# Performance work log

Hardware: AMD Instinct MI355X
Metric: run time of the kernel (lower is better)

The kernel has to match this reference:

```python
import jax, jax.numpy as jnp
import numpy as np
from jax import lax

B, C, H, W = 32, 128, 64, 64
K, KH, KW = 4, 3, 3
STRIDE = (1, 1)
PAD = [(1, 1), (1, 1)]


def setup_inputs() -> dict:
    key = jax.random.key(0)
    k1, k2, k3, k4 = jax.random.split(key, 4)
    x = jax.random.normal(k1, (B, C, H, W), dtype=jnp.float32)
    kernels = jax.random.normal(k2, (K, C, C, KH, KW), dtype=jnp.float32)
    fc_w = jax.random.normal(k3, (K, C), dtype=jnp.float32) * (1.0 / np.sqrt(C))
    fc_b = jax.random.normal(k4, (K,), dtype=jnp.float32) * 0.01
    return {"x": x, "kernels": kernels, "fc_w": fc_w, "fc_b": fc_b}


def reference(x, kernels, fc_w, fc_b):
    b, c, h, w = x.shape
    # DynamicRoutingLayer: GAP -> Linear -> sigmoid, then softmax over kernels
    pooled = x.mean(axis=(2, 3))                      # [B, C]
    coeffs = jax.nn.sigmoid(pooled @ fc_w.T + fc_b)   # [B, K]
    coeffs = jax.nn.softmax(coeffs, axis=1)
    # Per-sample mixed kernels: [B, C_out, C_in, kh, kw]
    dyn_k = jnp.einsum('bk,klmij->blmij', coeffs, kernels)
    # Batched per-sample conv via grouped conv: groups = batch
    xg = x.reshape(1, b * c, h, w)
    wg = dyn_k.reshape(b * c, c, KH, KW)
    out = lax.conv_general_dilated(
        xg, wg, window_strides=STRIDE, padding=PAD,
        dimension_numbers=('NCHW', 'OIHW', 'NCHW'),
        feature_group_count=b)
    return out.reshape(b, c, out.shape[2], out.shape[3])
```

## Files before the change

### kernel.cpp

```cpp
#include <hip/hip_runtime.h>
#include <math.h>

typedef __attribute__((ext_vector_type(8))) short s16x8;
typedef __attribute__((ext_vector_type(4))) float f32x4;
typedef __attribute__((ext_vector_type(4))) unsigned int u32x4;

#define CCH 128
#define BSZ 32

static __device__ inline unsigned short f2bf(float f) {
    unsigned u = __float_as_uint(f);
    unsigned r = (u + 0x7FFFu + ((u >> 16) & 1u)) >> 16;
    return (unsigned short)r;
}

static __device__ inline unsigned cvtpk(float lo, float hi) {
    unsigned r;
    asm("v_cvt_pk_bf16_f32 %0, %1, %2" : "=v"(r) : "v"(lo), "v"(hi));
    return r;
}

__global__ __launch_bounds__(256) void pool_kernel(const float* __restrict__ x,
                                                   float* __restrict__ pooled) {
    int blk = blockIdx.x;
    const float4* x4 = (const float4*)(x + (size_t)blk * 4096);
    int t = threadIdx.x;
    float s = 0.f;
#pragma unroll
    for (int j = 0; j < 4; ++j) {
        float4 v = x4[j * 256 + t];
        s += v.x + v.y + v.z + v.w;
    }
#pragma unroll
    for (int off = 32; off; off >>= 1) s += __shfl_xor(s, off, 64);
    __shared__ float red[4];
    if ((t & 63) == 0) red[t >> 6] = s;
    __syncthreads();
    if (t == 0) {
        float tot = red[0] + red[1] + red[2] + red[3];
        pooled[blk] = tot * (1.0f / 4096.0f);
    }
}

__global__ __launch_bounds__(128) void coeff_kernel(const float* __restrict__ pooled,
                                                    const float* __restrict__ fc_w,
                                                    const float* __restrict__ fc_b,
                                                    float* __restrict__ coeffs) {
    int t = threadIdx.x;
    int b = t >> 2, k = t & 3;
    const float4* p4 = (const float4*)(pooled + b * CCH);
    const float4* w4 = (const float4*)(fc_w + k * CCH);
    float dot = fc_b[k];
#pragma unroll
    for (int j = 0; j < 32; ++j) {
        float4 a = p4[j], w = w4[j];
        dot += a.x * w.x + a.y * w.y + a.z * w.z + a.w * w.w;
    }
    float s = 1.0f / (1.0f + expf(-dot));
    float m = s;
    m = fmaxf(m, __shfl_xor(m, 1, 64));
    m = fmaxf(m, __shfl_xor(m, 2, 64));
    float e = expf(s - m);
    float sum = e;
    sum += __shfl_xor(sum, 1, 64);
    sum += __shfl_xor(sum, 2, 64);
    coeffs[t] = e / sum;
}

__global__ __launch_bounds__(256) void mix_kernel(const float* __restrict__ kernels,
                                                  const float* __restrict__ coeffs,
                                                  unsigned short* __restrict__ wmix) {
    extern __shared__ float klds[];
    int bid = blockIdx.x;
    int bq = bid & 15;
    int rest = bid >> 4;
    int cog = rest & 7, cc = rest >> 3;
    int t = threadIdx.x;

    const int KSTR = CCH * CCH * 9;
    for (int s = t; s < 4 * 16 * 288; s += 256) {
        int k = s / 4608;
        int rem = s - k * 4608;
        int co = rem / 288;
        int i = rem - co * 288;
        klds[k * 4624 + co * 289 + i] =
            kernels[(size_t)k * KSTR + ((size_t)(cog * 16 + co) * CCH + cc * 32) * 9 + i];
    }
    __syncthreads();

    int wr = cog >> 2, mt = cog & 3;
#pragma unroll
    for (int jb = 0; jb < 2; ++jb) {
        int b = bq + jb * 16;
        float cf0 = coeffs[b * 4 + 0];
        float cf1 = coeffs[b * 4 + 1];
        float cf2 = coeffs[b * 4 + 2];
        float cf3 = coeffs[b * 4 + 3];
        for (int s = t; s < 576; s += 256) {
            int lane = s & 63;
            int tj = s >> 6;
            int dy = tj / 3, dx = tj - dy * 3;
            int col = lane & 15;
            int ci8 = (lane >> 4) * 8;
            unsigned short vals[8];
#pragma unroll
            for (int e = 0; e < 8; ++e) {
                int idx = col * 289 + (ci8 + e) * 9 + dy * 3 + dx;
                float v = cf0 * klds[idx]
                        + cf1 * klds[4624 + idx]
                        + cf2 * klds[2 * 4624 + idx]
                        + cf3 * klds[3 * 4624 + idx];
                vals[e] = f2bf(v);
            }
            int p = cc * 3 + dy;
            size_t off = (size_t)b * 147456
                       + ((size_t)((p * 3 + dx) * 2 + wr) * 4 + mt) * 512 + (size_t)lane * 8;
            *(s16x8*)&wmix[off] = *(const s16x8*)vals;
        }
    }
}

__global__ __launch_bounds__(512, 4) void conv_kernel(const float* __restrict__ x,
                                                      const unsigned short* __restrict__ wmix,
                                                      float* __restrict__ out) {
    __shared__ unsigned short xs[4 * 66 * 40];

    int bid = blockIdx.x;
    int b = bid & 31, ytile = bid >> 5;
    int y0 = ytile * 2;
    int t = threadIdx.x;
    int l = t & 63, w = t >> 6;
    int wr = w >> 2;
    int wc = (w >> 1) & 1;
    int wn = w & 1;
    int l15 = l & 15, g = l >> 4;

    const unsigned short* wb = wmix + (size_t)b * 147456;

    if (t < 160) {
        int row = t / 40;
        int colsel = (t / 20) & 1;
        int cpart = t % 20;
        *(unsigned*)&xs[(row * 66 + colsel * 65) * 40 + cpart * 2] = 0u;
    }

#pragma unroll
    for (int i = 0; i < 2; ++i) {
        int slot = w + i * 8;
        int row = slot >> 2, colhi = slot & 3;
        int gx = colhi * 16 + l15;
        int gy = y0 + row - 1;
        float v[8];
#pragma unroll
        for (int j = 0; j < 8; ++j) v[j] = 0.f;
        if ((unsigned)gy < 64u) {
            const float* xp = x + (((size_t)b * CCH + g * 8) * 64 + gy) * 64 + gx;
#pragma unroll
            for (int j = 0; j < 8; ++j) v[j] = xp[(size_t)j * 4096];
        }
        unsigned pw[4];
#pragma unroll
        for (int j = 0; j < 4; ++j) pw[j] = cvtpk(v[2 * j], v[2 * j + 1]);
        u32x4 q; q[0] = pw[0]; q[1] = pw[1]; q[2] = pw[2]; q[3] = pw[3];
        *(u32x4*)&xs[(size_t)(row * 66 + gx + 1) * 40 + g * 8] = q;
    }
    __syncthreads();

    f32x4 acc[4][2] = {};
    float xv[2][8];
    unsigned pk[2][4];

    for (int cc = 0; cc < 4; ++cc) {
        s16x8 a[4], n[4];
        {
            const unsigned short* wt = wb + ((size_t)((cc * 3) * 3) * 2 + wr) * 2048 + (size_t)l * 8;
#pragma unroll
            for (int mt = 0; mt < 4; ++mt) a[mt] = *(const s16x8*)(wt + mt * 512);
        }
        if (cc < 3) {
#pragma unroll
            for (int i = 0; i < 2; ++i) {
                int slot = w + i * 8;
                int row = slot >> 2, colhi = slot & 3;
                int gx = colhi * 16 + l15;
                int gy = y0 + row - 1;
#pragma unroll
                for (int j = 0; j < 8; ++j) xv[i][j] = 0.f;
                if ((unsigned)gy < 64u) {
                    const float* xp = x + (((size_t)b * CCH + (cc + 1) * 32 + g * 8) * 64 + gy) * 64 + gx;
#pragma unroll
                    for (int j = 0; j < 8; ++j) xv[i][j] = xp[(size_t)j * 4096];
                }
            }
        }
#pragma unroll
        for (int tap = 0; tap < 9; ++tap) {
            int dy = tap / 3, dx = tap - dy * 3;
            if (tap < 8) {
                int tap2 = tap + 1;
                int dy2 = tap2 / 3, dx2 = tap2 - dy2 * 3;
                const unsigned short* wt = wb + ((size_t)((cc * 3 + dy2) * 3 + dx2) * 2 + wr) * 2048
                                              + (size_t)l * 8;
#pragma unroll
                for (int mt = 0; mt < 4; ++mt) n[mt] = *(const s16x8*)(wt + mt * 512);
            }
            int xrow = wc + dy;
            s16x8 b0 = *(const s16x8*)&xs[(size_t)(xrow * 66 + wn * 32 + l15 + dx) * 40 + g * 8];
            s16x8 b1 = *(const s16x8*)&xs[(size_t)(xrow * 66 + wn * 32 + 16 + l15 + dx) * 40 + g * 8];
#pragma unroll
            for (int mt = 0; mt < 4; ++mt) {
                acc[mt][0] = __builtin_amdgcn_mfma_f32_16x16x32_bf16(a[mt], b0, acc[mt][0], 0, 0, 0);
                acc[mt][1] = __builtin_amdgcn_mfma_f32_16x16x32_bf16(a[mt], b1, acc[mt][1], 0, 0, 0);
            }
            if (tap < 8) {
#pragma unroll
                for (int mt = 0; mt < 4; ++mt) a[mt] = n[mt];
            }
        }
        if (cc < 3) {
#pragma unroll
            for (int i = 0; i < 2; ++i)
#pragma unroll
                for (int j = 0; j < 4; ++j)
                    pk[i][j] = cvtpk(xv[i][2 * j], xv[i][2 * j + 1]);
        }
        __syncthreads();
        if (cc < 3) {
#pragma unroll
            for (int i = 0; i < 2; ++i) {
                int slot = w + i * 8;
                int row = slot >> 2, colhi = slot & 3;
                int gx = colhi * 16 + l15;
                u32x4 q; q[0] = pk[i][0]; q[1] = pk[i][1]; q[2] = pk[i][2]; q[3] = pk[i][3];
                *(u32x4*)&xs[(size_t)(row * 66 + gx + 1) * 40 + g * 8] = q;
            }
            __syncthreads();
        }
    }

    int gy = y0 + wc;
#pragma unroll
    for (int mt = 0; mt < 4; ++mt)
#pragma unroll
        for (int ntl = 0; ntl < 2; ++ntl) {
            int gxo = (wn * 2 + ntl) * 16 + l15;
#pragma unroll
            for (int j = 0; j < 4; ++j) {
                int co = wr * 64 + mt * 16 + g * 4 + j;
                out[(((size_t)b * CCH + co) * 64 + gy) * 64 + gxo] = acc[mt][ntl][j];
            }
        }
}

extern "C" void kernel_launch(void* const* d_in, const int* in_sizes, int n_in,
                              void* d_out, int out_size, void* d_ws, size_t ws_size,
                              hipStream_t stream) {
    const float* x       = (const float*)d_in[0];
    const float* kernels = (const float*)d_in[1];
    const float* fc_w    = (const float*)d_in[2];
    const float* fc_b    = (const float*)d_in[3];
    float* out = (float*)d_out;

    float* pooled = (float*)d_ws;
    float* coeffs = pooled + BSZ * CCH;
    unsigned short* wmix = (unsigned short*)((char*)d_ws + 32768);

    hipFuncSetAttribute((const void*)mix_kernel,
                        hipFuncAttributeMaxDynamicSharedMemorySize, 73984);

    pool_kernel<<<BSZ * CCH, 256, 0, stream>>>(x, pooled);
    coeff_kernel<<<1, 128, 0, stream>>>(pooled, fc_w, fc_b, coeffs);
    mix_kernel<<<512, 256, 73984, stream>>>(kernels, coeffs, wmix);
    conv_kernel<<<1024, 512, 0, stream>>>(x, wmix, out);
}
```

Before: 94.36 us.

## Enlarge conv tile to four rows with 1024 threads and double-buffered LDS

The conv kernel now computes four output rows per block with 16 waves instead of two rows with 8, so each staged input halo (6 rows instead of 4) is shared by more outputs. The shared-memory input tile is double-buffered, which removes one of the two barriers per channel chunk because the next chunk can be written while the current one is read. The cost is larger LDS use per block, fewer blocks, and 1024-thread workgroups that may limit occupancy. Each wave also still reloads weights from global memory per tap.

```diff
diff --git a/kernel.cpp b/kernel.cpp
--- a/kernel.cpp
+++ b/kernel.cpp
@@ -4,6 +4,7 @@
 typedef __attribute__((ext_vector_type(8))) short s16x8;
 typedef __attribute__((ext_vector_type(4))) float f32x4;
 typedef __attribute__((ext_vector_type(4))) unsigned int u32x4;
+typedef __attribute__((ext_vector_type(2))) unsigned int u32x2;
 
 #define CCH 128
 #define BSZ 32
@@ -120,78 +121,79 @@
     }
 }
 
-__global__ __launch_bounds__(512, 4) void conv_kernel(const float* __restrict__ x,
-                                                      const unsigned short* __restrict__ wmix,
-                                                      float* __restrict__ out) {
-    __shared__ unsigned short xs[4 * 66 * 40];
+__global__ __launch_bounds__(1024, 4) void conv_kernel(const float* __restrict__ x,
+                                                       const unsigned short* __restrict__ wmix,
+                                                       float* __restrict__ out) {
+    __shared__ unsigned short xs[2][6 * 66 * 40];
 
     int bid = blockIdx.x;
     int b = bid & 31, ytile = bid >> 5;
-    int y0 = ytile * 2;
+    int y0 = ytile * 4;
     int t = threadIdx.x;
     int l = t & 63, w = t >> 6;
-    int wr = w >> 2;
-    int wc = (w >> 1) & 1;
-    int wn = w & 1;
+    int wr = w >> 3, wc = (w >> 1) & 3, wn = w & 1;
     int l15 = l & 15, g = l >> 4;
 
     const unsigned short* wb = wmix + (size_t)b * 147456;
 
-    if (t < 160) {
-        int row = t / 40;
-        int colsel = (t / 20) & 1;
-        int cpart = t % 20;
-        *(unsigned*)&xs[(row * 66 + colsel * 65) * 40 + cpart * 2] = 0u;
-    }
-
-#pragma unroll
-    for (int i = 0; i < 2; ++i) {
-        int slot = w + i * 8;
-        int row = slot >> 2, colhi = slot & 3;
-        int gx = colhi * 16 + l15;
-        int gy = y0 + row - 1;
-        float v[8];
-#pragma unroll
-        for (int j = 0; j < 8; ++j) v[j] = 0.f;
+    if (t < 480) {
+        int buf = t / 240;
+        int r = t - buf * 240;
+        int row = r / 40;
+        int colsel = (r / 20) & 1;
+        int cpart = r % 20;
+        *(unsigned*)&xs[buf][(row * 66 + colsel * 65) * 40 + cpart * 2] = 0u;
+    }
+
+    int hrow[3], hgx[3], hg[3], hh[3];
+#pragma unroll
+    for (int k = 0; k < 3; ++k) {
+        int h = t + k * 1024;
+        int slot = h >> 7, r7 = h & 127;
+        hrow[k] = slot >> 2;
+        hgx[k] = (slot & 3) * 16 + (r7 & 15);
+        hg[k] = (r7 >> 4) & 3;
+        hh[k] = (r7 >> 6) & 1;
+    }
+
+#pragma unroll
+    for (int k = 0; k < 3; ++k) {
+        int gy = y0 + hrow[k] - 1;
+        float v0 = 0.f, v1 = 0.f, v2 = 0.f, v3 = 0.f;
         if ((unsigned)gy < 64u) {
-            const float* xp = x + (((size_t)b * CCH + g * 8) * 64 + gy) * 64 + gx;
-#pragma unroll
-            for (int j = 0; j < 8; ++j) v[j] = xp[(size_t)j * 4096];
-        }
-        unsigned pw[4];
-#pragma unroll
-        for (int j = 0; j < 4; ++j) pw[j] = cvtpk(v[2 * j], v[2 * j + 1]);
-        u32x4 q; q[0] = pw[0]; q[1] = pw[1]; q[2] = pw[2]; q[3] = pw[3];
-        *(u32x4*)&xs[(size_t)(row * 66 + gx + 1) * 40 + g * 8] = q;
+            const float* xp = x + (((size_t)b * CCH + hg[k] * 8 + hh[k] * 4) * 64 + gy) * 64 + hgx[k];
+            v0 = xp[0]; v1 = xp[4096]; v2 = xp[2 * 4096]; v3 = xp[3 * 4096];
+        }
+        u32x2 q; q[0] = cvtpk(v0, v1); q[1] = cvtpk(v2, v3);
+        *(u32x2*)&xs[0][(size_t)(hrow[k] * 66 + hgx[k] + 1) * 40 + hg[k] * 8 + hh[k] * 4] = q;
     }
     __syncthreads();
 
     f32x4 acc[4][2] = {};
-    float xv[2][8];
-    unsigned pk[2][4];
+    float xv[3][4];
 
     for (int cc = 0; cc < 4; ++cc) {
-        s16x8 a[4], n[4];
+        const unsigned short* xcur = xs[cc & 1];
+        unsigned short* xnxt = xs[(cc + 1) & 1];
+
+        if (cc < 3) {
+#pragma unroll
+            for (int k = 0; k < 3; ++k) {
+                int gy = y0 + hrow[k] - 1;
+                xv[k][0] = 0.f; xv[k][1] = 0.f; xv[k][2] = 0.f; xv[k][3] = 0.f;
+                if ((unsigned)gy < 64u) {
+                    const float* xp = x + (((size_t)b * CCH + (cc + 1) * 32 + hg[k] * 8 + hh[k] * 4) * 64 + gy) * 64 + hgx[k];
+                    xv[k][0] = xp[0]; xv[k][1] = xp[4096];
+                    xv[k][2] = xp[2 * 4096]; xv[k][3] = xp[3 * 4096];
+                }
+            }
+        }
+
+        s16x8 a[4], an[4];
         {
-            const unsigned short* wt = wb + ((size_t)((cc * 3) * 3) * 2 + wr) * 2048 + (size_t)l * 8;
+            const unsigned short* wt = wb + ((size_t)((cc * 3) * 3 * 2 + wr) * 4) * 512 + (size_t)l * 8;
 #pragma unroll
             for (int mt = 0; mt < 4; ++mt) a[mt] = *(const s16x8*)(wt + mt * 512);
-        }
-        if (cc < 3) {
-#pragma unroll
-            for (int i = 0; i < 2; ++i) {
-                int slot = w + i * 8;
-                int row = slot >> 2, colhi = slot & 3;
-                int gx = colhi * 16 + l15;
-                int gy = y0 + row - 1;
-#pragma unroll
-                for (int j = 0; j < 8; ++j) xv[i][j] = 0.f;
-                if ((unsigned)gy < 64u) {
-                    const float* xp = x + (((size_t)b * CCH + (cc + 1) * 32 + g * 8) * 64 + gy) * 64 + gx;
-#pragma unroll
-                    for (int j = 0; j < 8; ++j) xv[i][j] = xp[(size_t)j * 4096];
-                }
-            }
         }
 #pragma unroll
         for (int tap = 0; tap < 9; ++tap) {
@@ -199,14 +201,15 @@
             if (tap < 8) {
                 int tap2 = tap + 1;
                 int dy2 = tap2 / 3, dx2 = tap2 - dy2 * 3;
-                const unsigned short* wt = wb + ((size_t)((cc * 3 + dy2) * 3 + dx2) * 2 + wr) * 2048
-                                              + (size_t)l * 8;
-#pragma unroll
-                for (int mt = 0; mt < 4; ++mt) n[mt] = *(const s16x8*)(wt + mt * 512);
+                const unsigned short* wt2 = wb + ((size_t)(((cc * 3 + dy2) * 3 + dx2) * 2 + wr) * 4) * 512
+                                               + (size_t)l * 8;
+#pragma unroll
+                for (int mt = 0; mt < 4; ++mt) an[mt] = *(const s16x8*)(wt2 + mt * 512);
             }
             int xrow = wc + dy;
-            s16x8 b0 = *(const s16x8*)&xs[(size_t)(xrow * 66 + wn * 32 + l15 + dx) * 40 + g * 8];
-            s16x8 b1 = *(const s16x8*)&xs[(size_t)(xrow * 66 + wn * 32 + 16 + l15 + dx) * 40 + g * 8];
+            int cb = wn * 32 + dx;
+            s16x8 b0 = *(const s16x8*)&xcur[(size_t)(xrow * 66 + cb + l15) * 40 + g * 8];
+            s16x8 b1 = *(const s16x8*)&xcur[(size_t)(xrow * 66 + cb + 16 + l15) * 40 + g * 8];
 #pragma unroll
             for (int mt = 0; mt < 4; ++mt) {
                 acc[mt][0] = __builtin_amdgcn_mfma_f32_16x16x32_bf16(a[mt], b0, acc[mt][0], 0, 0, 0);
@@ -214,28 +217,18 @@
             }
             if (tap < 8) {
 #pragma unroll
-                for (int mt = 0; mt < 4; ++mt) a[mt] = n[mt];
-            }
-        }
+                for (int mt = 0; mt < 4; ++mt) a[mt] = an[mt];
+            }
+        }
+
         if (cc < 3) {
 #pragma unroll
-            for (int i = 0; i < 2; ++i)
-#pragma unroll
-                for (int j = 0; j < 4; ++j)
-                    pk[i][j] = cvtpk(xv[i][2 * j], xv[i][2 * j + 1]);
+            for (int k = 0; k < 3; ++k) {
+                u32x2 q; q[0] = cvtpk(xv[k][0], xv[k][1]); q[1] = cvtpk(xv[k][2], xv[k][3]);
+                *(u32x2*)&xnxt[(size_t)(hrow[k] * 66 + hgx[k] + 1) * 40 + hg[k] * 8 + hh[k] * 4] = q;
+            }
         }
         __syncthreads();
-        if (cc < 3) {
-#pragma unroll
-            for (int i = 0; i < 2; ++i) {
-                int slot = w + i * 8;
-                int row = slot >> 2, colhi = slot & 3;
-                int gx = colhi * 16 + l15;
-                u32x4 q; q[0] = pk[i][0]; q[1] = pk[i][1]; q[2] = pk[i][2]; q[3] = pk[i][3];
-                *(u32x4*)&xs[(size_t)(row * 66 + gx + 1) * 40 + g * 8] = q;
-            }
-            __syncthreads();
-        }
     }
 
     int gy = y0 + wc;
@@ -271,5 +264,5 @@
     pool_kernel<<<BSZ * CCH, 256, 0, stream>>>(x, pooled);
     coeff_kernel<<<1, 128, 0, stream>>>(pooled, fc_w, fc_b, coeffs);
     mix_kernel<<<512, 256, 73984, stream>>>(kernels, coeffs, wmix);
-    conv_kernel<<<1024, 512, 0, stream>>>(x, wmix, out);
-}
+    conv_kernel<<<512, 1024, 0, stream>>>(x, wmix, out);
+}
```

Result: faster. 91.67 us (-2.8%).
